# Kernel optimization log

Hardware: AMD Instinct MI355X
Metric: run time of the kernel (lower is better)

Reference implementation:

```python
import jax, jax.numpy as jnp
import numpy as np

NU = 50000   # num user nodes
NI = 50000   # num item nodes
E = 1600000  # edges per relation
DIN = 256    # in_features
H = 8        # n_heads
F = 64       # out_features per head (hidden = H*F = 512)
NEG_SLOPE = 0.2


def setup_inputs() -> dict:
    key = jax.random.key(0)
    ks = jax.random.split(key, 14)
    wscale = 0.05
    return {
        "x_user": jax.random.normal(ks[0], (NU, DIN), jnp.float32),
        "x_item": jax.random.normal(ks[1], (NI, DIN), jnp.float32),
        "Wv": jax.random.normal(ks[2], (3, DIN, H * F), jnp.float32) * wscale,
        "bv": jax.random.normal(ks[3], (3, H * F), jnp.float32) * wscale,
        "Wq": jax.random.normal(ks[4], (3, H * F, H), jnp.float32) * wscale,
        "bq": jax.random.normal(ks[5], (3, H), jnp.float32) * wscale,
        "Wk": jax.random.normal(ks[6], (3, H * F, H), jnp.float32) * wscale,
        "bk": jax.random.normal(ks[7], (3, H), jnp.float32) * wscale,
        "src1": jax.random.randint(ks[8], (E,), 0, NU, jnp.int32),   # user -> item
        "dst1": jax.random.randint(ks[9], (E,), 0, NI, jnp.int32),
        "src2": jax.random.randint(ks[10], (E,), 0, NI, jnp.int32),  # item -> user
        "dst2": jax.random.randint(ks[11], (E,), 0, NU, jnp.int32),
        "src3": jax.random.randint(ks[12], (E,), 0, NU, jnp.int32),  # user -> user
        "dst3": jax.random.randint(ks[13], (E,), 0, NU, jnp.int32),
    }


def _gat_relation(x_src, x_dst, Wv, bv, Wq, bq, Wk, bk, src, dst, n_dst):
    # linear_v on src and dst node features: [N, H*F]
    h_src = x_src @ Wv + bv
    h_dst = x_dst @ Wv + bv
    q = h_dst @ Wq + bq  # [Nd, H] per-head query logit
    k = h_src @ Wk + bk  # [Ns, H] per-head key logit
    # fused_gsddmm: gather to edges, leaky_relu, segment softmax over dst
    e = jax.nn.leaky_relu(q[dst] + k[src], NEG_SLOPE)  # [E, H]
    m = jax.ops.segment_max(e, dst, num_segments=n_dst)  # [Nd, H]
    m = jnp.where(jnp.isfinite(m), m, jnp.zeros_like(m))
    ex = jnp.exp(e - m[dst])
    denom = jax.ops.segment_sum(ex, dst, num_segments=n_dst)  # [Nd, H]
    attn = ex / jnp.maximum(denom[dst], 1e-9)  # [E, H]
    # gspmm: attention-weighted scatter-sum of src features into dst
    hs = h_src.reshape(-1, H, F)  # [Ns, H, F]
    agg = jax.ops.segment_sum(attn[:, :, None] * hs[src], dst, num_segments=n_dst)  # [Nd, H, F]
    return agg.mean(axis=1)  # torch.mean(h, dim=1) -> [Nd, F]


def reference(x_user, x_item, Wv, bv, Wq, bq, Wk, bk, src1, dst1, src2, dst2, src3, dst3):
    # relation 0: user -> item
    out_item = _gat_relation(x_user, x_item, Wv[0], bv[0], Wq[0], bq[0], Wk[0], bk[0], src1, dst1, NI)
    # relations 1 (item -> user) and 2 (user -> user) both target user: mean over relations
    r1 = _gat_relation(x_item, x_user, Wv[1], bv[1], Wq[1], bq[1], Wk[1], bk[1], src2, dst2, NU)
    r2 = _gat_relation(x_user, x_user, Wv[2], bv[2], Wq[2], bq[2], Wk[2], bk[2], src3, dst3, NU)
    out_user = (r1 + r2) / 2.0
    return out_user, out_item
```

## Files before the change

kernel.cpp:

```cpp
#include <hip/hip_runtime.h>

typedef unsigned short u16;
typedef __attribute__((ext_vector_type(4))) float f32x4;
typedef __attribute__((ext_vector_type(8))) short s16x8;

#define NND 50000
#define EDG 1600000
#define NBK 391
#define TOTB (3 * NBK)
#define TS 4096

__device__ __forceinline__ u16 f2b(float f) {
  union { float f; unsigned u; } c; c.f = f;
  unsigned r = c.u + 0x7fff + ((c.u >> 16) & 1);
  return (u16)(r >> 16);
}
__device__ __forceinline__ float b2f(u16 b) {
  union { float f; unsigned u; } c; c.u = ((unsigned)b) << 16; return c.f;
}

__global__ void k_zero(int* p, int n) {
  int i = blockIdx.x * 256 + threadIdx.x;
  if (i < n) p[i] = 0;
}

__global__ void k_prepw(const float* __restrict__ Wv, u16* __restrict__ Wt) {
  int tid = blockIdx.x * 256 + threadIdx.x;
  if (tid < 3 * 512 * 256) {
    int r = tid / (512 * 256); int rem = tid - r * 512 * 256;
    int n = rem >> 8; int kk = rem & 255;
    Wt[tid] = f2b(Wv[((size_t)r * 256 + kk) * 512 + n]);
  }
}

__global__ void k_fusew(const float* __restrict__ Wv, const float* __restrict__ bv,
                        const float* __restrict__ Wq, const float* __restrict__ bq,
                        const float* __restrict__ Wk, const float* __restrict__ bk,
                        float* __restrict__ FW, float* __restrict__ FB) {
  int tid = blockIdx.x * 256 + threadIdx.x;
  if (tid < 3 * 16 * 256) {
    int r = tid >> 12, o = (tid >> 8) & 15, kk = tid & 255;
    const float* wv = Wv + ((size_t)r * 256 + kk) * 512;
    const float* wqk = (o < 8) ? (Wq + r * 512 * 8 + o) : (Wk + r * 512 * 8 + (o - 8));
    float s = 0.f;
    for (int j = 0; j < 512; j++) s += wv[j] * wqk[j * 8];
    FW[tid] = s;
  }
  if (tid < 48) {
    int r = tid / 16, o = tid % 16;
    const float* wqk = (o < 8) ? (Wq + r * 512 * 8 + o) : (Wk + r * 512 * 8 + (o - 8));
    const float* bvp = bv + r * 512;
    float s = (o < 8) ? bq[r * 8 + o] : bk[r * 8 + (o - 8)];
    for (int j = 0; j < 512; j++) s += bvp[j] * wqk[j * 8];
    FB[tid] = s;
  }
}

__global__ void kb_count(const int* __restrict__ d1, const int* __restrict__ d2,
                         const int* __restrict__ d3, int* __restrict__ BC) {
  __shared__ int h[NBK];
  int tid = threadIdx.x;
  int r = blockIdx.y;
  const int* d = (r == 0) ? d1 : (r == 1) ? d2 : d3;
  for (int b = tid; b < NBK; b += 256) h[b] = 0;
  __syncthreads();
  for (int e = blockIdx.x * 256 + tid; e < EDG; e += 256 * gridDim.x)
    atomicAdd(&h[d[e] >> 7], 1);
  __syncthreads();
  for (int b = tid; b < NBK; b += 256)
    if (h[b]) atomicAdd(&BC[r * NBK + b], h[b]);
}

__global__ void kb_scan(const int* __restrict__ BC, int* __restrict__ BB,
                        int* __restrict__ BCUR, int* __restrict__ rp) {
  __shared__ int a[2][2048];
  int t = threadIdx.x;
  a[0][t]        = (t < TOTB) ? BC[t] : 0;
  a[0][t + 1024] = (t + 1024 < TOTB) ? BC[t + 1024] : 0;
  __syncthreads();
  int s = 0;
  for (int off = 1; off < 2048; off <<= 1) {
    int v0 = a[s][t];        if (t >= off) v0 += a[s][t - off];
    int v1 = a[s][t + 1024]; if (t + 1024 >= off) v1 += a[s][t + 1024 - off];
    __syncthreads();
    a[s ^ 1][t] = v0; a[s ^ 1][t + 1024] = v1;
    __syncthreads();
    s ^= 1;
  }
  if (t < TOTB)        { int e = a[s][t] - BC[t];               BB[t] = e;        BCUR[t] = e; }
  if (t + 1024 < TOTB) { int e = a[s][t + 1024] - BC[t + 1024]; BB[t + 1024] = e; BCUR[t + 1024] = e; }
  if (t == 0) rp[3 * NND] = 3 * EDG;
}

__global__ void __launch_bounds__(256) kb_scatter(
    const int* __restrict__ s1, const int* __restrict__ d1,
    const int* __restrict__ s2, const int* __restrict__ d2,
    const int* __restrict__ s3, const int* __restrict__ d3,
    int* __restrict__ BCUR, unsigned* __restrict__ pairs) {
  __shared__ int h[NBK];
  __shared__ int bbase[NBK];
  int tid = threadIdx.x;
  int r = blockIdx.y;
  const int* dp = (r == 0) ? d1 : (r == 1) ? d2 : d3;
  const int* sp = (r == 0) ? s1 : (r == 1) ? s2 : s3;
  int e0 = blockIdx.x * TS;
  int n = EDG - e0; if (n > TS) n = TS;
  for (int b = tid; b < NBK; b += 256) h[b] = 0;
  __syncthreads();
  int eb[16]; unsigned ev[16];
#pragma unroll
  for (int k = 0; k < 16; k++) {
    int i = k * 256 + tid;
    if (i < n) {
      int d = dp[e0 + i], ss = sp[e0 + i];
      eb[k] = d >> 7;
      ev[k] = ((unsigned)(d & 127) << 16) | (unsigned)ss;
      atomicAdd(&h[eb[k]], 1);
    } else eb[k] = -1;
  }
  __syncthreads();
  for (int b = tid; b < NBK; b += 256) {
    int c = h[b];
    bbase[b] = c ? atomicAdd(&BCUR[r * NBK + b], c) : 0;
  }
  __syncthreads();
  for (int b = tid; b < NBK; b += 256) h[b] = 0;
  __syncthreads();
#pragma unroll
  for (int k = 0; k < 16; k++) {
    if (eb[k] >= 0) {
      int off = atomicAdd(&h[eb[k]], 1);
      pairs[bbase[eb[k]] + off] = ev[k];
    }
  }
}

__global__ void __launch_bounds__(256) kb_build(
    const unsigned* __restrict__ pairs, const int* __restrict__ BB,
    const int* __restrict__ BC, int* __restrict__ rp, int* __restrict__ csrc) {
  __shared__ int cntl[128];
  __shared__ int sc[128];
  __shared__ int curl[128];
  int t = threadIdx.x;
  int r = blockIdx.y, bx = blockIdx.x;
  int bin = r * NBK + bx;
  int base = BB[bin], cnt = BC[bin];
  int node0 = bx << 7;
  int nloc = NND - node0; if (nloc > 128) nloc = 128;
  if (t < 128) cntl[t] = 0;
  __syncthreads();
  for (int i = t; i < cnt; i += 256)
    atomicAdd(&cntl[pairs[base + i] >> 16], 1);
  __syncthreads();
  if (t < 128) sc[t] = cntl[t];
  __syncthreads();
  for (int off = 1; off < 128; off <<= 1) {
    int v = 0;
    if (t < 128) { v = sc[t]; if (t >= off) v += sc[t - off]; }
    __syncthreads();
    if (t < 128) sc[t] = v;
    __syncthreads();
  }
  if (t < 128) {
    int excl = sc[t] - cntl[t];
    if (t < nloc) rp[r * NND + node0 + t] = base + excl;
    curl[t] = base + excl;
  }
  __syncthreads();
  for (int i = t; i < cnt; i += 256) {
    unsigned v = pairs[base + i];
    int p = atomicAdd(&curl[v >> 16], 1);
    csrc[p] = (int)(v & 0xFFFFu);
  }
}

__global__ void __launch_bounds__(256) k_gemm(const float* __restrict__ A, const u16* __restrict__ Bt,
                                              const float* __restrict__ bias, u16* __restrict__ C, int M) {
  __shared__ u16 sA[128 * 40];
  __shared__ u16 sB[128 * 40];
  int tid = threadIdx.x;
  int lane = tid & 63, wid = tid >> 6;
  int wm = wid >> 1, wn = wid & 1;
  int l15 = lane & 15, l4 = lane >> 4;
  int m0 = blockIdx.x * 128, n0 = blockIdx.y * 128;
  f32x4 acc[4][4] = {};
  for (int ko = 0; ko < 256; ko += 32) {
#pragma unroll
    for (int p = 0; p < 2; p++) {
      int idx = p * 256 + tid;
      int row = idx >> 2, seg = idx & 3;
      int gm = m0 + row; if (gm >= M) gm = M - 1;
      float4 a0 = *(const float4*)(A + (size_t)gm * 256 + ko + seg * 8);
      float4 a1 = *(const float4*)(A + (size_t)gm * 256 + ko + seg * 8 + 4);
      s16x8 av;
      av[0] = (short)f2b(a0.x); av[1] = (short)f2b(a0.y);
      av[2] = (short)f2b(a0.z); av[3] = (short)f2b(a0.w);
      av[4] = (short)f2b(a1.x); av[5] = (short)f2b(a1.y);
      av[6] = (short)f2b(a1.z); av[7] = (short)f2b(a1.w);
      *(s16x8*)&sA[row * 40 + seg * 8] = av;
      *(s16x8*)&sB[row * 40 + seg * 8] = *(const s16x8*)(Bt + (n0 + row) * 256 + ko + seg * 8);
    }
    __syncthreads();
    s16x8 af[4], bf[4];
#pragma unroll
    for (int i = 0; i < 4; i++) af[i] = *(const s16x8*)&sA[(wm * 64 + i * 16 + l15) * 40 + l4 * 8];
#pragma unroll
    for (int j = 0; j < 4; j++) bf[j] = *(const s16x8*)&sB[(wn * 64 + j * 16 + l15) * 40 + l4 * 8];
#pragma unroll
    for (int i = 0; i < 4; i++)
#pragma unroll
      for (int j = 0; j < 4; j++)
        acc[i][j] = __builtin_amdgcn_mfma_f32_16x16x32_bf16(af[i], bf[j], acc[i][j], 0, 0, 0);
    __syncthreads();
  }
#pragma unroll
  for (int j = 0; j < 4; j++) {
    int n = n0 + wn * 64 + j * 16 + l15;
    float bb = bias[n];
    int tpos = ((n & 63) << 3) + (n >> 6);
#pragma unroll
    for (int i = 0; i < 4; i++) {
      int mb = m0 + wm * 64 + i * 16 + l4 * 4;
#pragma unroll
      for (int r = 0; r < 4; r++) {
        int m = mb + r;
        if (m < M) C[(size_t)m * 512 + tpos] = f2b(acc[i][j][r] + bb);
      }
    }
  }
}

__global__ void __launch_bounds__(256) k_qk_u(
    const float* __restrict__ x, const float* __restrict__ FW,
    const float* __restrict__ FB, float* __restrict__ K0,
    float* __restrict__ Q1, float* __restrict__ Q2,
    float* __restrict__ K2, int N) {
  int lane = threadIdx.x & 63, wid = threadIdx.x >> 6;
  int stride = gridDim.x * 4;
  for (int row = blockIdx.x * 4 + wid; row < N; row += stride) {
    float4 xv = *(const float4*)(x + (size_t)row * 256 + lane * 4);
    {
      float p[16];
#pragma unroll
      for (int c = 0; c < 16; c++) {
        const float4 wv = *(const float4*)(FW + (size_t)(8 + c) * 256 + lane * 4);
        p[c] = xv.x * wv.x + xv.y * wv.y + xv.z * wv.z + xv.w * wv.w;
      }
#pragma unroll
      for (int off = 1; off < 64; off <<= 1)
#pragma unroll
        for (int c = 0; c < 16; c++) p[c] += __shfl_xor(p[c], off, 64);
      if (lane == 0) {
#pragma unroll
        for (int c = 0; c < 8; c++) K0[row * 8 + c] = p[c] + FB[8 + c];
#pragma unroll
        for (int c = 0; c < 8; c++) Q1[row * 8 + c] = p[8 + c] + FB[16 + c];
      }
    }
    {
      float p[16];
#pragma unroll
      for (int c = 0; c < 16; c++) {
        const float4 wv = *(const float4*)(FW + (size_t)(32 + c) * 256 + lane * 4);
        p[c] = xv.x * wv.x + xv.y * wv.y + xv.z * wv.z + xv.w * wv.w;
      }
#pragma unroll
      for (int off = 1; off < 64; off <<= 1)
#pragma unroll
        for (int c = 0; c < 16; c++) p[c] += __shfl_xor(p[c], off, 64);
      if (lane == 0) {
#pragma unroll
        for (int c = 0; c < 8; c++) Q2[row * 8 + c] = p[c] + FB[32 + c];
#pragma unroll
        for (int c = 0; c < 8; c++) K2[row * 8 + c] = p[8 + c] + FB[40 + c];
      }
    }
  }
}

__global__ void __launch_bounds__(256) k_qk_i(
    const float* __restrict__ x, const float* __restrict__ FW,
    const float* __restrict__ FB, float* __restrict__ Q0,
    float* __restrict__ K1, int N) {
  int lane = threadIdx.x & 63, wid = threadIdx.x >> 6;
  int stride = gridDim.x * 4;
  for (int row = blockIdx.x * 4 + wid; row < N; row += stride) {
    float4 xv = *(const float4*)(x + (size_t)row * 256 + lane * 4);
    float p[16];
#pragma unroll
    for (int c = 0; c < 16; c++) {
      const float4 wv = *(const float4*)(FW + (size_t)((c < 8) ? c : (16 + c)) * 256 + lane * 4);
      p[c] = xv.x * wv.x + xv.y * wv.y + xv.z * wv.z + xv.w * wv.w;
    }
#pragma unroll
    for (int off = 1; off < 64; off <<= 1)
#pragma unroll
      for (int c = 0; c < 16; c++) p[c] += __shfl_xor(p[c], off, 64);
    if (lane == 0) {
#pragma unroll
      for (int c = 0; c < 8; c++) Q0[row * 8 + c] = p[c] + FB[c];
#pragma unroll
      for (int c = 0; c < 8; c++) K1[row * 8 + c] = p[8 + c] + FB[24 + c];
    }
  }
}

__global__ void __launch_bounds__(256) k_edge(const int* __restrict__ rp, const int* __restrict__ csrc,
                       const float* __restrict__ q, const float* __restrict__ k,
                       const u16* __restrict__ hs, float* __restrict__ out,
                       float scale, int accum) {
  __shared__ float exw[4][64 * 8];
  __shared__ int sarr[4][64];
  __shared__ float sd[4][8];
  __shared__ float sacc[4][64];
  int lane = threadIdx.x & 63, w = threadIdx.x >> 6;
  int dst = blockIdx.x * 2 + (w >> 1);
  int half = w & 1;
  int beg = rp[dst];
  int deg = rp[dst + 1] - beg;
  int hlen = (deg + 1) >> 1;
  int s0 = half ? hlen : 0;
  int s1 = half ? deg : hlen;
  float qv[8];
  {
    float4 q0 = *(const float4*)(q + dst * 8);
    float4 q1 = *(const float4*)(q + dst * 8 + 4);
    qv[0] = q0.x; qv[1] = q0.y; qv[2] = q0.z; qv[3] = q0.w;
    qv[4] = q1.x; qv[5] = q1.y; qv[6] = q1.z; qv[7] = q1.w;
  }
  float dsum[8] = {0, 0, 0, 0, 0, 0, 0, 0};
  for (int i = s0 + lane; i < s1; i += 64) {
    int s = csrc[beg + i];
    float4 k0 = *(const float4*)(k + s * 8);
    float4 k1 = *(const float4*)(k + s * 8 + 4);
    float kv[8] = {k0.x, k0.y, k0.z, k0.w, k1.x, k1.y, k1.z, k1.w};
#pragma unroll
    for (int h = 0; h < 8; h++) {
      float e = qv[h] + kv[h];
      e = e > 0.f ? e : 0.2f * e;
      dsum[h] += exp2f(e * 1.44269504f);
    }
  }
#pragma unroll
  for (int off = 1; off < 64; off <<= 1)
#pragma unroll
    for (int h = 0; h < 8; h++) dsum[h] += __shfl_xor(dsum[h], off, 64);
  if (lane == 0) {
#pragma unroll
    for (int h = 0; h < 8; h++) sd[w][h] = dsum[h];
  }
  __syncthreads();
  float rden[8];
#pragma unroll
  for (int h = 0; h < 8; h++) {
    float tot = sd[w][h] + sd[w ^ 1][h];
    rden[h] = tot > 0.f ? 1.f / tot : 0.f;
  }

  float acc8[8] = {0, 0, 0, 0, 0, 0, 0, 0};
  for (int base = s0; base < s1; base += 64) {
    int i = base + lane;
    int nn = min(64, s1 - base);
    if (i < s1) {
      int s = csrc[beg + i];
      sarr[w][lane] = s;
      float4 k0 = *(const float4*)(k + s * 8);
      float4 k1 = *(const float4*)(k + s * 8 + 4);
      float kv[8] = {k0.x, k0.y, k0.z, k0.w, k1.x, k1.y, k1.z, k1.w};
#pragma unroll
      for (int h = 0; h < 8; h++) {
        float e = qv[h] + kv[h];
        e = e > 0.f ? e : 0.2f * e;
        exw[w][lane * 8 + h] = exp2f(e * 1.44269504f) * rden[h];
      }
    }
    __asm__ __volatile__("s_waitcnt lgkmcnt(0)" ::: "memory");
    for (int j = 0; j < nn; j++) {
      int s = sarr[w][j];
      s16x8 hv = *(const s16x8*)(hs + (size_t)s * 512 + lane * 8);
      float4 e0 = *(const float4*)&exw[w][j * 8];
      float4 e1 = *(const float4*)&exw[w][j * 8 + 4];
      acc8[0] += e0.x * b2f((u16)hv[0]);
      acc8[1] += e0.y * b2f((u16)hv[1]);
      acc8[2] += e0.z * b2f((u16)hv[2]);
      acc8[3] += e0.w * b2f((u16)hv[3]);
      acc8[4] += e1.x * b2f((u16)hv[4]);
      acc8[5] += e1.y * b2f((u16)hv[5]);
      acc8[6] += e1.z * b2f((u16)hv[6]);
      acc8[7] += e1.w * b2f((u16)hv[7]);
    }
  }
  float acc = ((acc8[0] + acc8[1]) + (acc8[2] + acc8[3])) + ((acc8[4] + acc8[5]) + (acc8[6] + acc8[7]));
  acc *= scale;
  sacc[w][lane] = acc;
  __syncthreads();
  if (half == 0) {
    float tot = sacc[w][lane] + sacc[w + 1][lane];
    if (accum) out[dst * 64 + lane] += tot;
    else out[dst * 64 + lane] = tot;
  }
}

extern "C" void kernel_launch(void* const* d_in, const int* in_sizes, int n_in,
                              void* d_out, int out_size, void* d_ws, size_t ws_size,
                              hipStream_t stream) {
  const float* xu = (const float*)d_in[0];
  const float* xi = (const float*)d_in[1];
  const float* Wv = (const float*)d_in[2];
  const float* bv = (const float*)d_in[3];
  const float* Wq = (const float*)d_in[4];
  const float* bq = (const float*)d_in[5];
  const float* Wk = (const float*)d_in[6];
  const float* bk = (const float*)d_in[7];
  const int* src1 = (const int*)d_in[8];
  const int* dst1 = (const int*)d_in[9];
  const int* src2 = (const int*)d_in[10];
  const int* dst2 = (const int*)d_in[11];
  const int* src3 = (const int*)d_in[12];
  const int* dst3 = (const int*)d_in[13];
  float* out_user = (float*)d_out;
  float* out_item = out_user + (size_t)NND * 64;

  char* w = (char*)d_ws;
  auto alloc = [&](size_t sz) -> char* {
    char* p = w; w += (sz + 255) & ~(size_t)255; return p;
  };
  u16* H    = (u16*)alloc((size_t)NND * 512 * 2);
  u16* WT   = (u16*)alloc((size_t)3 * 512 * 256 * 2);
  float* FW = (float*)alloc((size_t)3 * 16 * 256 * 4);
  float* FB = (float*)alloc((size_t)3 * 16 * 4);
  float* Q0 = (float*)alloc((size_t)NND * 8 * 4);
  float* K0 = (float*)alloc((size_t)NND * 8 * 4);
  float* Q1 = (float*)alloc((size_t)NND * 8 * 4);
  float* K1 = (float*)alloc((size_t)NND * 8 * 4);
  float* Q2 = (float*)alloc((size_t)NND * 8 * 4);
  float* K2 = (float*)alloc((size_t)NND * 8 * 4);
  int* ROWPTR = (int*)alloc(((size_t)3 * NND + 1) * 4);
  int* BC   = (int*)alloc(TOTB * 4);
  int* BB   = (int*)alloc(TOTB * 4);
  int* BCUR = (int*)alloc(TOTB * 4);
  int* CSRC = (int*)alloc((size_t)3 * EDG * 4);
  unsigned* PAIRS = (unsigned*)H;
  (void)ws_size; (void)n_in; (void)in_sizes; (void)out_size;

  k_zero<<<(TOTB + 255) / 256, 256, 0, stream>>>(BC, TOTB);
  kb_count<<<dim3(256, 3), 256, 0, stream>>>(dst1, dst2, dst3, BC);
  kb_scan<<<1, 1024, 0, stream>>>(BC, BB, BCUR, ROWPTR);
  kb_scatter<<<dim3((EDG + TS - 1) / TS, 3), 256, 0, stream>>>(src1, dst1, src2, dst2, src3, dst3, BCUR, PAIRS);
  kb_build<<<dim3(NBK, 3), 256, 0, stream>>>(PAIRS, BB, BC, ROWPTR, CSRC);

  k_prepw<<<(3 * 512 * 256 + 255) / 256, 256, 0, stream>>>(Wv, WT);
  k_fusew<<<48, 256, 0, stream>>>(Wv, bv, Wq, bq, Wk, bk, FW, FB);

  k_qk_u<<<1024, 256, 0, stream>>>(xu, FW, FB, K0, Q1, Q2, K2, NND);
  k_qk_i<<<1024, 256, 0, stream>>>(xi, FW, FB, Q0, K1, NND);

  dim3 gg((NND + 127) / 128, 4);
  k_gemm<<<gg, 256, 0, stream>>>(xu, WT,                 bv,        H, NND);
  k_edge<<<NND / 2, 256, 0, stream>>>(ROWPTR,           CSRC, Q0, K0, H, out_item, 0.125f,  0);
  k_gemm<<<gg, 256, 0, stream>>>(xi, WT + 512 * 256,     bv + 512,  H, NND);
  k_edge<<<NND / 2, 256, 0, stream>>>(ROWPTR + NND,     CSRC, Q1, K1, H, out_user, 0.0625f, 0);
  k_gemm<<<gg, 256, 0, stream>>>(xu, WT + 2 * 512 * 256, bv + 1024, H, NND);
  k_edge<<<NND / 2, 256, 0, stream>>>(ROWPTR + 2 * NND, CSRC, Q2, K2, H, out_user, 0.0625f, 1);
}
```

Measured before the change: 1.251 ms.

## Fuse softmax denominator into aggregation pass and sort CSR rows by source

The edge kernel no longer runs a separate first pass to compute the softmax denominators. It now accumulates unnormalized exp-weighted features together with per-head exp sums in one pass, then divides by the denominator at the end. This removes one full round of csrc and k gathers per edge. A new kernel sorts each destination's source list with warp-level bitonic sorts (rows with more than 128 entries are left unsorted), aiming for better gather locality and a deterministic order. That adds one extra launch and some preprocessing work.

```diff
diff --git a/kernel.cpp b/kernel.cpp
--- a/kernel.cpp
+++ b/kernel.cpp
@@ -171,6 +171,54 @@
     unsigned v = pairs[base + i];
     int p = atomicAdd(&curl[v >> 16], 1);
     csrc[p] = (int)(v & 0xFFFFu);
+  }
+}
+
+__global__ void __launch_bounds__(256) k_sortrows(const int* __restrict__ rp, int* __restrict__ csrc) {
+  int lane = threadIdx.x & 63, w = threadIdx.x >> 6;
+  int node = blockIdx.x * 4 + w;
+  if (node >= 3 * NND) return;
+  int beg = rp[node];
+  int deg = rp[node + 1] - beg;
+  if (deg <= 1) return;
+  if (deg <= 64) {
+    int v = (lane < deg) ? csrc[beg + lane] : 0x7FFFFFFF;
+#pragma unroll
+    for (int k = 2; k <= 64; k <<= 1) {
+#pragma unroll
+      for (int j = k >> 1; j > 0; j >>= 1) {
+        int p = __shfl_xor(v, j, 64);
+        bool up = ((lane & k) == 0) || (k == 64);
+        bool keepmin = (((lane & j) == 0) == up);
+        v = keepmin ? min(v, p) : max(v, p);
+      }
+    }
+    if (lane < deg) csrc[beg + lane] = v;
+  } else if (deg <= 128) {
+    int i0 = lane, i1 = lane + 64;
+    int v0 = (i0 < deg) ? csrc[beg + i0] : 0x7FFFFFFF;
+    int v1 = (i1 < deg) ? csrc[beg + i1] : 0x7FFFFFFF;
+#pragma unroll
+    for (int k = 2; k <= 128; k <<= 1) {
+#pragma unroll
+      for (int j = k >> 1; j > 0; j >>= 1) {
+        if (j == 64) {
+          bool up = ((i0 & k) == 0) || (k == 128);
+          int mn = min(v0, v1), mx = max(v0, v1);
+          v0 = up ? mn : mx; v1 = up ? mx : mn;
+        } else {
+          int p0 = __shfl_xor(v0, j, 64);
+          int p1 = __shfl_xor(v1, j, 64);
+          bool keep0 = ((lane & j) == 0);
+          bool up0 = ((i0 & k) == 0) || (k == 128);
+          bool up1 = ((i1 & k) == 0) || (k == 128);
+          v0 = (keep0 == up0) ? min(v0, p0) : max(v0, p0);
+          v1 = (keep0 == up1) ? min(v1, p1) : max(v1, p1);
+        }
+      }
+    }
+    if (i0 < deg) csrc[beg + i0] = v0;
+    if (i1 < deg) csrc[beg + i1] = v1;
   }
 }
 
@@ -328,36 +376,8 @@
     qv[0] = q0.x; qv[1] = q0.y; qv[2] = q0.z; qv[3] = q0.w;
     qv[4] = q1.x; qv[5] = q1.y; qv[6] = q1.z; qv[7] = q1.w;
   }
+  float num[8] = {0, 0, 0, 0, 0, 0, 0, 0};
   float dsum[8] = {0, 0, 0, 0, 0, 0, 0, 0};
-  for (int i = s0 + lane; i < s1; i += 64) {
-    int s = csrc[beg + i];
-    float4 k0 = *(const float4*)(k + s * 8);
-    float4 k1 = *(const float4*)(k + s * 8 + 4);
-    float kv[8] = {k0.x, k0.y, k0.z, k0.w, k1.x, k1.y, k1.z, k1.w};
-#pragma unroll
-    for (int h = 0; h < 8; h++) {
-      float e = qv[h] + kv[h];
-      e = e > 0.f ? e : 0.2f * e;
-      dsum[h] += exp2f(e * 1.44269504f);
-    }
-  }
-#pragma unroll
-  for (int off = 1; off < 64; off <<= 1)
-#pragma unroll
-    for (int h = 0; h < 8; h++) dsum[h] += __shfl_xor(dsum[h], off, 64);
-  if (lane == 0) {
-#pragma unroll
-    for (int h = 0; h < 8; h++) sd[w][h] = dsum[h];
-  }
-  __syncthreads();
-  float rden[8];
-#pragma unroll
-  for (int h = 0; h < 8; h++) {
-    float tot = sd[w][h] + sd[w ^ 1][h];
-    rden[h] = tot > 0.f ? 1.f / tot : 0.f;
-  }
-
-  float acc8[8] = {0, 0, 0, 0, 0, 0, 0, 0};
   for (int base = s0; base < s1; base += 64) {
     int i = base + lane;
     int nn = min(64, s1 - base);
@@ -371,7 +391,9 @@
       for (int h = 0; h < 8; h++) {
         float e = qv[h] + kv[h];
         e = e > 0.f ? e : 0.2f * e;
-        exw[w][lane * 8 + h] = exp2f(e * 1.44269504f) * rden[h];
+        float wgt = exp2f(e * 1.44269504f);
+        exw[w][lane * 8 + h] = wgt;
+        dsum[h] += wgt;
       }
     }
     __asm__ __volatile__("s_waitcnt lgkmcnt(0)" ::: "memory");
@@ -380,17 +402,32 @@
       s16x8 hv = *(const s16x8*)(hs + (size_t)s * 512 + lane * 8);
       float4 e0 = *(const float4*)&exw[w][j * 8];
       float4 e1 = *(const float4*)&exw[w][j * 8 + 4];
-      acc8[0] += e0.x * b2f((u16)hv[0]);
-      acc8[1] += e0.y * b2f((u16)hv[1]);
-      acc8[2] += e0.z * b2f((u16)hv[2]);
-      acc8[3] += e0.w * b2f((u16)hv[3]);
-      acc8[4] += e1.x * b2f((u16)hv[4]);
-      acc8[5] += e1.y * b2f((u16)hv[5]);
-      acc8[6] += e1.z * b2f((u16)hv[6]);
-      acc8[7] += e1.w * b2f((u16)hv[7]);
-    }
-  }
-  float acc = ((acc8[0] + acc8[1]) + (acc8[2] + acc8[3])) + ((acc8[4] + acc8[5]) + (acc8[6] + acc8[7]));
+      num[0] += e0.x * b2f((u16)hv[0]);
+      num[1] += e0.y * b2f((u16)hv[1]);
+      num[2] += e0.z * b2f((u16)hv[2]);
+      num[3] += e0.w * b2f((u16)hv[3]);
+      num[4] += e1.x * b2f((u16)hv[4]);
+      num[5] += e1.y * b2f((u16)hv[5]);
+      num[6] += e1.z * b2f((u16)hv[6]);
+      num[7] += e1.w * b2f((u16)hv[7]);
+    }
+  }
+#pragma unroll
+  for (int off = 1; off < 64; off <<= 1)
+#pragma unroll
+    for (int h = 0; h < 8; h++) dsum[h] += __shfl_xor(dsum[h], off, 64);
+  if (lane == 0) {
+#pragma unroll
+    for (int h = 0; h < 8; h++) sd[w][h] = dsum[h];
+  }
+  __syncthreads();
+  float acc = 0.f;
+#pragma unroll
+  for (int h = 0; h < 8; h++) {
+    float tot = sd[w][h] + sd[w ^ 1][h];
+    float rden = tot > 0.f ? 1.f / tot : 0.f;
+    acc += num[h] * rden;
+  }
   acc *= scale;
   sacc[w][lane] = acc;
   __syncthreads();
@@ -448,6 +485,7 @@
   kb_scan<<<1, 1024, 0, stream>>>(BC, BB, BCUR, ROWPTR);
   kb_scatter<<<dim3((EDG + TS - 1) / TS, 3), 256, 0, stream>>>(src1, dst1, src2, dst2, src3, dst3, BCUR, PAIRS);
   kb_build<<<dim3(NBK, 3), 256, 0, stream>>>(PAIRS, BB, BC, ROWPTR, CSRC);
+  k_sortrows<<<(3 * NND + 3) / 4, 256, 0, stream>>>(ROWPTR, CSRC);
 
   k_prepw<<<(3 * 512 * 256 + 255) / 256, 256, 0, stream>>>(Wv, WT);
   k_fusew<<<48, 256, 0, stream>>>(Wv, bv, Wq, bq, Wk, bk, FW, FB);
```

Measured after the change: 1.274 ms. No clear change (+1.8%).

## Replace per-destination CSR edge kernel with 32-node bucket sweep sorted by source

Applied to the files above, without the earlier changes.

The CSR build is dropped in favour of buckets of 32 destination nodes. Within each bucket, edges are sorted by source range, with a staging pass through shared memory, to improve locality of the gathers. The edge kernel now handles one bucket per block: it accumulates the softmax denominators and the weighted feature sums with shared-memory atomics, broadcasting per-edge weights across the wave with readlane. This aims to raise occupancy and L2 reuse of source rows and remove the per-node load imbalance. In exchange it adds shared atomic contention and makes every lane perform an atomic add for each edge.

```diff
diff --git a/kernel.cpp b/kernel.cpp
--- a/kernel.cpp
+++ b/kernel.cpp
@@ -6,9 +6,11 @@
 
 #define NND 50000
 #define EDG 1600000
-#define NBK 391
-#define TOTB (3 * NBK)
+#define BKT 32
+#define NBK2 1563
+#define TOTB2 (3 * NBK2)
 #define TS 4096
+#define SBINS 128
 
 __device__ __forceinline__ u16 f2b(float f) {
   union { float f; unsigned u; } c; c.f = f;
@@ -58,38 +60,45 @@
 
 __global__ void kb_count(const int* __restrict__ d1, const int* __restrict__ d2,
                          const int* __restrict__ d3, int* __restrict__ BC) {
-  __shared__ int h[NBK];
+  __shared__ int h[NBK2];
   int tid = threadIdx.x;
   int r = blockIdx.y;
   const int* d = (r == 0) ? d1 : (r == 1) ? d2 : d3;
-  for (int b = tid; b < NBK; b += 256) h[b] = 0;
+  for (int b = tid; b < NBK2; b += 256) h[b] = 0;
   __syncthreads();
   for (int e = blockIdx.x * 256 + tid; e < EDG; e += 256 * gridDim.x)
-    atomicAdd(&h[d[e] >> 7], 1);
-  __syncthreads();
-  for (int b = tid; b < NBK; b += 256)
-    if (h[b]) atomicAdd(&BC[r * NBK + b], h[b]);
+    atomicAdd(&h[d[e] >> 5], 1);
+  __syncthreads();
+  for (int b = tid; b < NBK2; b += 256)
+    if (h[b]) atomicAdd(&BC[r * NBK2 + b], h[b]);
 }
 
 __global__ void kb_scan(const int* __restrict__ BC, int* __restrict__ BB,
-                        int* __restrict__ BCUR, int* __restrict__ rp) {
-  __shared__ int a[2][2048];
+                        int* __restrict__ BCUR) {
+  __shared__ int a[2][1024];
   int t = threadIdx.x;
-  a[0][t]        = (t < TOTB) ? BC[t] : 0;
-  a[0][t + 1024] = (t + 1024 < TOTB) ? BC[t + 1024] : 0;
+  int base = t * 8;
+  int v[8]; int run = 0;
+#pragma unroll
+  for (int i = 0; i < 8; i++) {
+    int x = (base + i < TOTB2) ? BC[base + i] : 0;
+    v[i] = run; run += x;
+  }
+  a[0][t] = run;
   __syncthreads();
   int s = 0;
-  for (int off = 1; off < 2048; off <<= 1) {
-    int v0 = a[s][t];        if (t >= off) v0 += a[s][t - off];
-    int v1 = a[s][t + 1024]; if (t + 1024 >= off) v1 += a[s][t + 1024 - off];
+  for (int off = 1; off < 1024; off <<= 1) {
+    int val = a[s][t]; if (t >= off) val += a[s][t - off];
     __syncthreads();
-    a[s ^ 1][t] = v0; a[s ^ 1][t + 1024] = v1;
+    a[s ^ 1][t] = val;
     __syncthreads();
     s ^= 1;
   }
-  if (t < TOTB)        { int e = a[s][t] - BC[t];               BB[t] = e;        BCUR[t] = e; }
-  if (t + 1024 < TOTB) { int e = a[s][t + 1024] - BC[t + 1024]; BB[t + 1024] = e; BCUR[t + 1024] = e; }
-  if (t == 0) rp[3 * NND] = 3 * EDG;
+  int texcl = a[s][t] - run;
+#pragma unroll
+  for (int i = 0; i < 8; i++) {
+    if (base + i < TOTB2) { int e = texcl + v[i]; BB[base + i] = e; BCUR[base + i] = e; }
+  }
 }
 
 __global__ void __launch_bounds__(256) kb_scatter(
@@ -97,15 +106,15 @@
     const int* __restrict__ s2, const int* __restrict__ d2,
     const int* __restrict__ s3, const int* __restrict__ d3,
     int* __restrict__ BCUR, unsigned* __restrict__ pairs) {
-  __shared__ int h[NBK];
-  __shared__ int bbase[NBK];
+  __shared__ int h[NBK2];
+  __shared__ int bbase[NBK2];
   int tid = threadIdx.x;
   int r = blockIdx.y;
   const int* dp = (r == 0) ? d1 : (r == 1) ? d2 : d3;
   const int* sp = (r == 0) ? s1 : (r == 1) ? s2 : s3;
   int e0 = blockIdx.x * TS;
   int n = EDG - e0; if (n > TS) n = TS;
-  for (int b = tid; b < NBK; b += 256) h[b] = 0;
+  for (int b = tid; b < NBK2; b += 256) h[b] = 0;
   __syncthreads();
   int eb[16]; unsigned ev[16];
 #pragma unroll
@@ -113,18 +122,18 @@
     int i = k * 256 + tid;
     if (i < n) {
       int d = dp[e0 + i], ss = sp[e0 + i];
-      eb[k] = d >> 7;
-      ev[k] = ((unsigned)(d & 127) << 16) | (unsigned)ss;
+      eb[k] = d >> 5;
+      ev[k] = ((unsigned)(d & 31) << 16) | (unsigned)ss;
       atomicAdd(&h[eb[k]], 1);
     } else eb[k] = -1;
   }
   __syncthreads();
-  for (int b = tid; b < NBK; b += 256) {
+  for (int b = tid; b < NBK2; b += 256) {
     int c = h[b];
-    bbase[b] = c ? atomicAdd(&BCUR[r * NBK + b], c) : 0;
-  }
-  __syncthreads();
-  for (int b = tid; b < NBK; b += 256) h[b] = 0;
+    bbase[b] = c ? atomicAdd(&BCUR[r * NBK2 + b], c) : 0;
+  }
+  __syncthreads();
+  for (int b = tid; b < NBK2; b += 256) h[b] = 0;
   __syncthreads();
 #pragma unroll
   for (int k = 0; k < 16; k++) {
@@ -135,43 +144,35 @@
   }
 }
 
-__global__ void __launch_bounds__(256) kb_build(
+__global__ void __launch_bounds__(256) kb_build2(
     const unsigned* __restrict__ pairs, const int* __restrict__ BB,
-    const int* __restrict__ BC, int* __restrict__ rp, int* __restrict__ csrc) {
-  __shared__ int cntl[128];
-  __shared__ int sc[128];
-  __shared__ int curl[128];
+    const int* __restrict__ BC, unsigned* __restrict__ cp) {
+  __shared__ int hist[SBINS];
+  __shared__ unsigned stg[2048];
   int t = threadIdx.x;
-  int r = blockIdx.y, bx = blockIdx.x;
-  int bin = r * NBK + bx;
+  int bin = blockIdx.y * NBK2 + blockIdx.x;
   int base = BB[bin], cnt = BC[bin];
-  int node0 = bx << 7;
-  int nloc = NND - node0; if (nloc > 128) nloc = 128;
-  if (t < 128) cntl[t] = 0;
+  if (cnt > 2048) {
+    for (int i = t; i < cnt; i += 256) cp[base + i] = pairs[base + i];
+    return;
+  }
+  for (int i = t; i < SBINS; i += 256) hist[i] = 0;
   __syncthreads();
   for (int i = t; i < cnt; i += 256)
-    atomicAdd(&cntl[pairs[base + i] >> 16], 1);
-  __syncthreads();
-  if (t < 128) sc[t] = cntl[t];
-  __syncthreads();
-  for (int off = 1; off < 128; off <<= 1) {
-    int v = 0;
-    if (t < 128) { v = sc[t]; if (t >= off) v += sc[t - off]; }
-    __syncthreads();
-    if (t < 128) sc[t] = v;
-    __syncthreads();
-  }
-  if (t < 128) {
-    int excl = sc[t] - cntl[t];
-    if (t < nloc) rp[r * NND + node0 + t] = base + excl;
-    curl[t] = base + excl;
+    atomicAdd(&hist[(pairs[base + i] & 0xFFFFu) >> 9], 1);
+  __syncthreads();
+  if (t == 0) {
+    int run = 0;
+    for (int b = 0; b < SBINS; b++) { int c = hist[b]; hist[b] = run; run += c; }
   }
   __syncthreads();
   for (int i = t; i < cnt; i += 256) {
-    unsigned v = pairs[base + i];
-    int p = atomicAdd(&curl[v >> 16], 1);
-    csrc[p] = (int)(v & 0xFFFFu);
-  }
+    unsigned p = pairs[base + i];
+    int b = (int)((p & 0xFFFFu) >> 9);
+    stg[atomicAdd(&hist[b], 1)] = p;
+  }
+  __syncthreads();
+  for (int i = t; i < cnt; i += 256) cp[base + i] = stg[i];
 }
 
 __global__ void __launch_bounds__(256) k_gemm(const float* __restrict__ A, const u16* __restrict__ Bt,
@@ -305,99 +306,88 @@
   }
 }
 
-__global__ void __launch_bounds__(256) k_edge(const int* __restrict__ rp, const int* __restrict__ csrc,
-                       const float* __restrict__ q, const float* __restrict__ k,
-                       const u16* __restrict__ hs, float* __restrict__ out,
-                       float scale, int accum) {
-  __shared__ float exw[4][64 * 8];
-  __shared__ int sarr[4][64];
-  __shared__ float sd[4][8];
-  __shared__ float sacc[4][64];
-  int lane = threadIdx.x & 63, w = threadIdx.x >> 6;
-  int dst = blockIdx.x * 2 + (w >> 1);
-  int half = w & 1;
-  int beg = rp[dst];
-  int deg = rp[dst + 1] - beg;
-  int hlen = (deg + 1) >> 1;
-  int s0 = half ? hlen : 0;
-  int s1 = half ? deg : hlen;
-  float qv[8];
-  {
-    float4 q0 = *(const float4*)(q + dst * 8);
-    float4 q1 = *(const float4*)(q + dst * 8 + 4);
-    qv[0] = q0.x; qv[1] = q0.y; qv[2] = q0.z; qv[3] = q0.w;
-    qv[4] = q1.x; qv[5] = q1.y; qv[6] = q1.z; qv[7] = q1.w;
-  }
-  float dsum[8] = {0, 0, 0, 0, 0, 0, 0, 0};
-  for (int i = s0 + lane; i < s1; i += 64) {
-    int s = csrc[beg + i];
-    float4 k0 = *(const float4*)(k + s * 8);
-    float4 k1 = *(const float4*)(k + s * 8 + 4);
+__global__ void __launch_bounds__(256) k_edge_sweep(
+    const unsigned* __restrict__ cp, const int* __restrict__ bb, const int* __restrict__ bc,
+    const float* __restrict__ q, const float* __restrict__ k,
+    const u16* __restrict__ hs, float* __restrict__ out,
+    float scale, int accum) {
+  __shared__ float acc[BKT][64];
+  __shared__ float qd[BKT][9];
+  __shared__ float den[BKT][9];
+  int tid = threadIdx.x;
+  int lane = tid & 63, w = tid >> 6;
+  int bx = blockIdx.x;
+  int base = bb[bx], cnt = bc[bx];
+  int node0 = bx * BKT;
+  for (int i = tid; i < BKT * 64; i += 256) acc[i >> 6][i & 63] = 0.f;
+  if (tid < BKT * 8) {
+    int dl = tid >> 3, h = tid & 7;
+    int row = node0 + dl;
+    qd[dl][h] = (row < NND) ? q[row * 8 + h] : 0.f;
+    den[dl][h] = 0.f;
+  }
+  __syncthreads();
+  for (int p = tid; p < cnt; p += 256) {
+    unsigned pr = cp[base + p];
+    int src = (int)(pr & 0xFFFFu), dl = (int)(pr >> 16);
+    float4 k0 = *(const float4*)(k + src * 8);
+    float4 k1 = *(const float4*)(k + src * 8 + 4);
     float kv[8] = {k0.x, k0.y, k0.z, k0.w, k1.x, k1.y, k1.z, k1.w};
 #pragma unroll
     for (int h = 0; h < 8; h++) {
-      float e = qv[h] + kv[h];
+      float e = qd[dl][h] + kv[h];
       e = e > 0.f ? e : 0.2f * e;
-      dsum[h] += exp2f(e * 1.44269504f);
-    }
-  }
-#pragma unroll
-  for (int off = 1; off < 64; off <<= 1)
-#pragma unroll
-    for (int h = 0; h < 8; h++) dsum[h] += __shfl_xor(dsum[h], off, 64);
-  if (lane == 0) {
-#pragma unroll
-    for (int h = 0; h < 8; h++) sd[w][h] = dsum[h];
-  }
-  __syncthreads();
-  float rden[8];
-#pragma unroll
-  for (int h = 0; h < 8; h++) {
-    float tot = sd[w][h] + sd[w ^ 1][h];
-    rden[h] = tot > 0.f ? 1.f / tot : 0.f;
-  }
-
-  float acc8[8] = {0, 0, 0, 0, 0, 0, 0, 0};
-  for (int base = s0; base < s1; base += 64) {
-    int i = base + lane;
-    int nn = min(64, s1 - base);
-    if (i < s1) {
-      int s = csrc[beg + i];
-      sarr[w][lane] = s;
-      float4 k0 = *(const float4*)(k + s * 8);
-      float4 k1 = *(const float4*)(k + s * 8 + 4);
+      atomicAdd(&den[dl][h], exp2f(e * 1.44269504f));
+    }
+  }
+  __syncthreads();
+  if (tid < BKT * 8) {
+    int dl = tid >> 3, h = tid & 7;
+    float v = den[dl][h];
+    den[dl][h] = v > 0.f ? 1.f / v : 0.f;
+  }
+  __syncthreads();
+  int nch = (cnt + 63) >> 6;
+  for (int c = w; c < nch; c += 4) {
+    int e0 = c * 64;
+    int nn = min(64, cnt - e0);
+    unsigned pr = 0u;
+    float wt[8] = {0, 0, 0, 0, 0, 0, 0, 0};
+    if (lane < nn) {
+      pr = cp[base + e0 + lane];
+      int src = (int)(pr & 0xFFFFu), dl = (int)(pr >> 16);
+      float4 k0 = *(const float4*)(k + src * 8);
+      float4 k1 = *(const float4*)(k + src * 8 + 4);
       float kv[8] = {k0.x, k0.y, k0.z, k0.w, k1.x, k1.y, k1.z, k1.w};
 #pragma unroll
       for (int h = 0; h < 8; h++) {
-        float e = qv[h] + kv[h];
+        float e = qd[dl][h] + kv[h];
         e = e > 0.f ? e : 0.2f * e;
-        exw[w][lane * 8 + h] = exp2f(e * 1.44269504f) * rden[h];
-      }
-    }
-    __asm__ __volatile__("s_waitcnt lgkmcnt(0)" ::: "memory");
+        wt[h] = exp2f(e * 1.44269504f) * den[dl][h];
+      }
+    }
     for (int j = 0; j < nn; j++) {
-      int s = sarr[w][j];
-      s16x8 hv = *(const s16x8*)(hs + (size_t)s * 512 + lane * 8);
-      float4 e0 = *(const float4*)&exw[w][j * 8];
-      float4 e1 = *(const float4*)&exw[w][j * 8 + 4];
-      acc8[0] += e0.x * b2f((u16)hv[0]);
-      acc8[1] += e0.y * b2f((u16)hv[1]);
-      acc8[2] += e0.z * b2f((u16)hv[2]);
-      acc8[3] += e0.w * b2f((u16)hv[3]);
-      acc8[4] += e1.x * b2f((u16)hv[4]);
-      acc8[5] += e1.y * b2f((u16)hv[5]);
-      acc8[6] += e1.z * b2f((u16)hv[6]);
-      acc8[7] += e1.w * b2f((u16)hv[7]);
-    }
-  }
-  float acc = ((acc8[0] + acc8[1]) + (acc8[2] + acc8[3])) + ((acc8[4] + acc8[5]) + (acc8[6] + acc8[7]));
-  acc *= scale;
-  sacc[w][lane] = acc;
-  __syncthreads();
-  if (half == 0) {
-    float tot = sacc[w][lane] + sacc[w + 1][lane];
-    if (accum) out[dst * 64 + lane] += tot;
-    else out[dst * 64 + lane] = tot;
+      unsigned prj = (unsigned)__builtin_amdgcn_readlane((int)pr, j);
+      int sj = (int)(prj & 0xFFFFu), dj = (int)(prj >> 16);
+      s16x8 hv = *(const s16x8*)(hs + (size_t)sj * 512 + lane * 8);
+      float partial = 0.f;
+#pragma unroll
+      for (int h = 0; h < 8; h++) {
+        float wj = __int_as_float(__builtin_amdgcn_readlane(__float_as_int(wt[h]), j));
+        partial += wj * b2f((u16)hv[h]);
+      }
+      atomicAdd(&acc[dj][lane], partial);
+    }
+  }
+  __syncthreads();
+  for (int i = 0; i < BKT / 4; i++) {
+    int dl = w * (BKT / 4) + i;
+    int row = node0 + dl;
+    if (row < NND) {
+      float v = acc[dl][lane] * scale;
+      if (accum) out[(size_t)row * 64 + lane] += v;
+      else out[(size_t)row * 64 + lane] = v;
+    }
   }
 }
 
@@ -435,19 +425,18 @@
   float* K1 = (float*)alloc((size_t)NND * 8 * 4);
   float* Q2 = (float*)alloc((size_t)NND * 8 * 4);
   float* K2 = (float*)alloc((size_t)NND * 8 * 4);
-  int* ROWPTR = (int*)alloc(((size_t)3 * NND + 1) * 4);
-  int* BC   = (int*)alloc(TOTB * 4);
-  int* BB   = (int*)alloc(TOTB * 4);
-  int* BCUR = (int*)alloc(TOTB * 4);
-  int* CSRC = (int*)alloc((size_t)3 * EDG * 4);
+  int* BC   = (int*)alloc(TOTB2 * 4);
+  int* BB   = (int*)alloc(TOTB2 * 4);
+  int* BCUR = (int*)alloc(TOTB2 * 4);
+  unsigned* CPAIRS = (unsigned*)alloc((size_t)3 * EDG * 4);
   unsigned* PAIRS = (unsigned*)H;
   (void)ws_size; (void)n_in; (void)in_sizes; (void)out_size;
 
-  k_zero<<<(TOTB + 255) / 256, 256, 0, stream>>>(BC, TOTB);
+  k_zero<<<(TOTB2 + 255) / 256, 256, 0, stream>>>(BC, TOTB2);
   kb_count<<<dim3(256, 3), 256, 0, stream>>>(dst1, dst2, dst3, BC);
-  kb_scan<<<1, 1024, 0, stream>>>(BC, BB, BCUR, ROWPTR);
+  kb_scan<<<1, 1024, 0, stream>>>(BC, BB, BCUR);
   kb_scatter<<<dim3((EDG + TS - 1) / TS, 3), 256, 0, stream>>>(src1, dst1, src2, dst2, src3, dst3, BCUR, PAIRS);
-  kb_build<<<dim3(NBK, 3), 256, 0, stream>>>(PAIRS, BB, BC, ROWPTR, CSRC);
+  kb_build2<<<dim3(NBK2, 3), 256, 0, stream>>>(PAIRS, BB, BC, CPAIRS);
 
   k_prepw<<<(3 * 512 * 256 + 255) / 256, 256, 0, stream>>>(Wv, WT);
   k_fusew<<<48, 256, 0, stream>>>(Wv, bv, Wq, bq, Wk, bk, FW, FB);
@@ -457,9 +446,9 @@
 
   dim3 gg((NND + 127) / 128, 4);
   k_gemm<<<gg, 256, 0, stream>>>(xu, WT,                 bv,        H, NND);
-  k_edge<<<NND / 2, 256, 0, stream>>>(ROWPTR,           CSRC, Q0, K0, H, out_item, 0.125f,  0);
+  k_edge_sweep<<<NBK2, 256, 0, stream>>>(CPAIRS, BB,            BC,            Q0, K0, H, out_item, 0.125f,  0);
   k_gemm<<<gg, 256, 0, stream>>>(xi, WT + 512 * 256,     bv + 512,  H, NND);
-  k_edge<<<NND / 2, 256, 0, stream>>>(ROWPTR + NND,     CSRC, Q1, K1, H, out_user, 0.0625f, 0);
+  k_edge_sweep<<<NBK2, 256, 0, stream>>>(CPAIRS, BB + NBK2,     BC + NBK2,     Q1, K1, H, out_user, 0.0625f, 0);
   k_gemm<<<gg, 256, 0, stream>>>(xu, WT + 2 * 512 * 256, bv + 1024, H, NND);
-  k_edge<<<NND / 2, 256, 0, stream>>>(ROWPTR + 2 * NND, CSRC, Q2, K2, H, out_user, 0.0625f, 1);
-}
+  k_edge_sweep<<<NBK2, 256, 0, stream>>>(CPAIRS, BB + 2 * NBK2, BC + 2 * NBK2, Q2, K2, H, out_user, 0.0625f, 1);
+}
```

New measurement: 2.602 ms. 2.08x slower.

## Fuse softmax denominator pass into aggregation and unroll gather loop by four

Applied to the files above, without the earlier changes.

Drops the separate first pass over edges that computed softmax denominators. Unnormalized exp weights are now accumulated alongside the numerator and divided at the end, which removes one read of csrc/k and one exp computation per edge. The inner gather loop is also unrolled by four with uint4 loads and bit-shift bf16 decoding, so more global loads are in flight at once. The cost is skipping max-subtraction, which the old code also skipped, and somewhat higher register use.

```diff
diff --git a/kernel.cpp b/kernel.cpp
--- a/kernel.cpp
+++ b/kernel.cpp
@@ -17,6 +17,17 @@
 }
 __device__ __forceinline__ float b2f(u16 b) {
   union { float f; unsigned u; } c; c.u = ((unsigned)b) << 16; return c.f;
+}
+
+__device__ __forceinline__ void accum8(float* num, uint4 u, float4 w0, float4 w1) {
+  num[0] += w0.x * __int_as_float((int)(u.x << 16));
+  num[1] += w0.y * __int_as_float((int)(u.x & 0xFFFF0000u));
+  num[2] += w0.z * __int_as_float((int)(u.y << 16));
+  num[3] += w0.w * __int_as_float((int)(u.y & 0xFFFF0000u));
+  num[4] += w1.x * __int_as_float((int)(u.z << 16));
+  num[5] += w1.y * __int_as_float((int)(u.z & 0xFFFF0000u));
+  num[6] += w1.z * __int_as_float((int)(u.w << 16));
+  num[7] += w1.w * __int_as_float((int)(u.w & 0xFFFF0000u));
 }
 
 __global__ void k_zero(int* p, int n) {
@@ -328,36 +339,8 @@
     qv[0] = q0.x; qv[1] = q0.y; qv[2] = q0.z; qv[3] = q0.w;
     qv[4] = q1.x; qv[5] = q1.y; qv[6] = q1.z; qv[7] = q1.w;
   }
+  float num[8] = {0, 0, 0, 0, 0, 0, 0, 0};
   float dsum[8] = {0, 0, 0, 0, 0, 0, 0, 0};
-  for (int i = s0 + lane; i < s1; i += 64) {
-    int s = csrc[beg + i];
-    float4 k0 = *(const float4*)(k + s * 8);
-    float4 k1 = *(const float4*)(k + s * 8 + 4);
-    float kv[8] = {k0.x, k0.y, k0.z, k0.w, k1.x, k1.y, k1.z, k1.w};
-#pragma unroll
-    for (int h = 0; h < 8; h++) {
-      float e = qv[h] + kv[h];
-      e = e > 0.f ? e : 0.2f * e;
-      dsum[h] += exp2f(e * 1.44269504f);
-    }
-  }
-#pragma unroll
-  for (int off = 1; off < 64; off <<= 1)
-#pragma unroll
-    for (int h = 0; h < 8; h++) dsum[h] += __shfl_xor(dsum[h], off, 64);
-  if (lane == 0) {
-#pragma unroll
-    for (int h = 0; h < 8; h++) sd[w][h] = dsum[h];
-  }
-  __syncthreads();
-  float rden[8];
-#pragma unroll
-  for (int h = 0; h < 8; h++) {
-    float tot = sd[w][h] + sd[w ^ 1][h];
-    rden[h] = tot > 0.f ? 1.f / tot : 0.f;
-  }
-
-  float acc8[8] = {0, 0, 0, 0, 0, 0, 0, 0};
   for (int base = s0; base < s1; base += 64) {
     int i = base + lane;
     int nn = min(64, s1 - base);
@@ -371,26 +354,52 @@
       for (int h = 0; h < 8; h++) {
         float e = qv[h] + kv[h];
         e = e > 0.f ? e : 0.2f * e;
-        exw[w][lane * 8 + h] = exp2f(e * 1.44269504f) * rden[h];
+        float wgt = exp2f(e * 1.44269504f);
+        exw[w][lane * 8 + h] = wgt;
+        dsum[h] += wgt;
       }
     }
     __asm__ __volatile__("s_waitcnt lgkmcnt(0)" ::: "memory");
-    for (int j = 0; j < nn; j++) {
+    int j = 0;
+    for (; j + 4 <= nn; j += 4) {
+      int sa = sarr[w][j], sb = sarr[w][j + 1], sc = sarr[w][j + 2], sdn = sarr[w][j + 3];
+      uint4 ua = *(const uint4*)(hs + (size_t)sa * 512 + lane * 8);
+      uint4 ub = *(const uint4*)(hs + (size_t)sb * 512 + lane * 8);
+      uint4 uc = *(const uint4*)(hs + (size_t)sc * 512 + lane * 8);
+      uint4 ud = *(const uint4*)(hs + (size_t)sdn * 512 + lane * 8);
+      float4 wa0 = *(const float4*)&exw[w][j * 8],       wa1 = *(const float4*)&exw[w][j * 8 + 4];
+      float4 wb0 = *(const float4*)&exw[w][j * 8 + 8],   wb1 = *(const float4*)&exw[w][j * 8 + 12];
+      float4 wc0 = *(const float4*)&exw[w][j * 8 + 16],  wc1 = *(const float4*)&exw[w][j * 8 + 20];
+      float4 wd0 = *(const float4*)&exw[w][j * 8 + 24],  wd1 = *(const float4*)&exw[w][j * 8 + 28];
+      accum8(num, ua, wa0, wa1);
+      accum8(num, ub, wb0, wb1);
+      accum8(num, uc, wc0, wc1);
+      accum8(num, ud, wd0, wd1);
+    }
+    for (; j < nn; j++) {
       int s = sarr[w][j];
-      s16x8 hv = *(const s16x8*)(hs + (size_t)s * 512 + lane * 8);
+      uint4 u = *(const uint4*)(hs + (size_t)s * 512 + lane * 8);
       float4 e0 = *(const float4*)&exw[w][j * 8];
       float4 e1 = *(const float4*)&exw[w][j * 8 + 4];
-      acc8[0] += e0.x * b2f((u16)hv[0]);
-      acc8[1] += e0.y * b2f((u16)hv[1]);
-      acc8[2] += e0.z * b2f((u16)hv[2]);
-      acc8[3] += e0.w * b2f((u16)hv[3]);
-      acc8[4] += e1.x * b2f((u16)hv[4]);
-      acc8[5] += e1.y * b2f((u16)hv[5]);
-      acc8[6] += e1.z * b2f((u16)hv[6]);
-      acc8[7] += e1.w * b2f((u16)hv[7]);
-    }
-  }
-  float acc = ((acc8[0] + acc8[1]) + (acc8[2] + acc8[3])) + ((acc8[4] + acc8[5]) + (acc8[6] + acc8[7]));
+      accum8(num, u, e0, e1);
+    }
+  }
+#pragma unroll
+  for (int off = 1; off < 64; off <<= 1)
+#pragma unroll
+    for (int h = 0; h < 8; h++) dsum[h] += __shfl_xor(dsum[h], off, 64);
+  if (lane == 0) {
+#pragma unroll
+    for (int h = 0; h < 8; h++) sd[w][h] = dsum[h];
+  }
+  __syncthreads();
+  float acc = 0.f;
+#pragma unroll
+  for (int h = 0; h < 8; h++) {
+    float tot = sd[w][h] + sd[w ^ 1][h];
+    float rden = tot > 0.f ? 1.f / tot : 0.f;
+    acc += num[h] * rden;
+  }
   acc *= scale;
   sacc[w][lane] = acc;
   __syncthreads();
```

Result: no change. 1.234 ms (-1.4%).
